# Performance work log

Hardware: AMD Instinct MI355X
Metric: run time of the kernel (lower is better)

## Reference

```python
import jax, jax.numpy as jnp
import numpy as np

D_MODEL = 1024
NUM_HEADS = 16
HEAD_DIM = D_MODEL // NUM_HEADS
B, S = 2, 2048


def setup_inputs() -> dict:
    key = jax.random.key(0)
    ks = jax.random.split(key, 10)
    sc = 1.0 / np.sqrt(D_MODEL)
    return {
        "x": jax.random.normal(ks[0], (B, S, D_MODEL), jnp.float32),
        "y": jax.random.normal(ks[1], (B, S, D_MODEL), jnp.float32),
        "Wkv": jax.random.normal(ks[2], (D_MODEL, 2 * D_MODEL), jnp.float32) * sc,
        "bkv": jax.random.normal(ks[3], (2 * D_MODEL,), jnp.float32) * 0.01,
        "Wq": jax.random.normal(ks[4], (D_MODEL, D_MODEL), jnp.float32) * sc,
        "bq": jax.random.normal(ks[5], (D_MODEL,), jnp.float32) * 0.01,
        "Wo": jax.random.normal(ks[6], (D_MODEL, D_MODEL), jnp.float32) * sc,
        "bo": jax.random.normal(ks[7], (D_MODEL,), jnp.float32) * 0.01,
    }


def reference(x, y, Wkv, bkv, Wq, bq, Wo, bo):
    b, s, d = x.shape
    # projections: kv from x (keys/values come from encoder side), q from y
    kv = x @ Wkv + bkv                      # [B, S, 2*d_model]
    q = y @ Wq + bq                         # [B, S, d_model]
    kv = kv.reshape(b, s, NUM_HEADS, 2 * HEAD_DIM).transpose(0, 2, 1, 3)  # [B,H,S,2*hd]
    q = q.reshape(b, s, NUM_HEADS, HEAD_DIM).transpose(0, 2, 1, 3)        # [B,H,S,hd]
    k, v = jnp.split(kv, 2, axis=-1)        # each [B,H,S,hd]
    scaled = jnp.einsum("bhqd,bhkd->bhqk", q, k) / np.sqrt(HEAD_DIM)      # [B,H,S,S]
    attention = jax.nn.softmax(scaled, axis=-1)
    values = jnp.einsum("bhqk,bhkd->bhqd", attention, v)                  # [B,H,S,hd]
    values = values.transpose(0, 2, 1, 3).reshape(b, s, d)                # [B,S,d_model]
    return values @ Wo + bo
```

## Files before the change

### kernel.cpp

```cpp
#include <hip/hip_runtime.h>
#include <hip/hip_bf16.h>

typedef __attribute__((ext_vector_type(8))) short short8;
typedef __attribute__((ext_vector_type(4))) short short4v;
typedef __attribute__((ext_vector_type(4))) float f32x4;
typedef __attribute__((ext_vector_type(16))) float f32x16;

#define B_  2
#define S_  2048
#define H_  16
#define HD_ 64
#define D_  1024
#define QSCALE 0.18033688f

__device__ __forceinline__ short f2bs(float f) {
  union { float f; unsigned u; } c; c.f = f;
  unsigned u = c.u;
  u += 0x7fffu + ((u >> 16) & 1u);
  return (short)(u >> 16);
}

__device__ __forceinline__ unsigned pack_bf16(float a, float b) {
  __hip_bfloat162 h = __float22bfloat162_rn(float2{a, b});
  return *reinterpret_cast<unsigned*>(&h);
}

__device__ __forceinline__ float fexp2(float x) {
#if __has_builtin(__builtin_amdgcn_exp2f)
  return __builtin_amdgcn_exp2f(x);
#else
  return exp2f(x);
#endif
}

__device__ __forceinline__ float frcp(float x) {
#if __has_builtin(__builtin_amdgcn_rcpf)
  return __builtin_amdgcn_rcpf(x);
#else
  return 1.0f / x;
#endif
}

#define GL2LDS(gp, lp) __builtin_amdgcn_global_load_lds( \
    (const __attribute__((address_space(1))) unsigned int*)(gp), \
    (__attribute__((address_space(3))) unsigned int*)(lp), 16, 0, 0)

__global__ __launch_bounds__(256)
void prep_kernel(const float* __restrict__ x, const float* __restrict__ y,
                 short* __restrict__ xb, short* __restrict__ yb,
                 const float* __restrict__ Wkv, short* __restrict__ Wkvt,
                 const float* __restrict__ Wq, short* __restrict__ Wqt,
                 const float* __restrict__ Wo, short* __restrict__ Wot) {
  __shared__ float tile[64][65];
  int bx = blockIdx.x;
  if (bx < 8192) {
    int i = bx * 256 + threadIdx.x;
    const float4* src; short4v* dst; int j;
    if (i < (1 << 20)) { src = (const float4*)x; dst = (short4v*)xb; j = i; }
    else               { src = (const float4*)y; dst = (short4v*)yb; j = i - (1 << 20); }
    float4 f = src[j];
    short4v o;
    o.x = f2bs(f.x); o.y = f2bs(f.y); o.z = f2bs(f.z); o.w = f2bs(f.w);
    dst[j] = o;
    return;
  }
  bx -= 8192;
  const float* in; short* out; int C, c0, r0;
  if (bx < 512)      { in = Wkv; out = Wkvt; C = 2048; c0 = (bx & 31) * 64; r0 = (bx >> 5) * 64; }
  else if (bx < 768) { bx -= 512; in = Wq; out = Wqt; C = 1024; c0 = (bx & 15) * 64; r0 = (bx >> 4) * 64; }
  else               { bx -= 768; in = Wo; out = Wot; C = 1024; c0 = (bx & 15) * 64; r0 = (bx >> 4) * 64; }
  const int tx = threadIdx.x & 63, ty = threadIdx.x >> 6;
#pragma unroll
  for (int i = 0; i < 16; ++i) {
    int r = ty + i * 4;
    tile[r][tx] = in[(size_t)(r0 + r) * C + c0 + tx];
  }
  __syncthreads();
#pragma unroll
  for (int i = 0; i < 16; ++i) {
    int r = ty + i * 4;
    out[(size_t)(c0 + r) * 1024 + r0 + tx] = f2bs(tile[tx][r]);
  }
}

template <int MODE>
__device__ __forceinline__ void gemm_body(const short* __restrict__ A, const short* __restrict__ Bt,
                                          const float* __restrict__ bias,
                                          void* __restrict__ out0, void* __restrict__ out1,
                                          int m0, int n0, int K, short* smem) {
  short* As_ = smem;
  short* Bs_ = smem + 8192;
  const int tid = threadIdx.x;
  const int w = tid >> 6, lane = tid & 63;
  const int q15 = lane & 15, quad = lane >> 4;
  const int wm = (w >> 1) * 64, wn = (w & 1) * 64;

  f32x4 acc[4][4];
#pragma unroll
  for (int i = 0; i < 4; ++i)
#pragma unroll
    for (int j = 0; j < 4; ++j) acc[i][j] = f32x4{0.f, 0.f, 0.f, 0.f};

  const int srow = w * 16 + (lane >> 2);
  const int gch  = (lane & 3) ^ ((lane >> 3) & 3);
  const short* Ag = A + (size_t)(m0 + srow) * K + gch * 8;
  const short* Bg = Bt + (size_t)(n0 + srow) * K + gch * 8;
  const int lof = srow * 32 + (lane & 3) * 8;

  GL2LDS(Ag,                  As_ + lof);
  GL2LDS(Ag + (size_t)64 * K, As_ + lof + 2048);
  GL2LDS(Bg,                  Bs_ + lof);
  GL2LDS(Bg + (size_t)64 * K, Bs_ + lof + 2048);

  const int NT = K >> 5;
  for (int kt = 0; kt < NT; ++kt) {
    __syncthreads();
    const short* Ac = As_ + (kt & 1) * 4096;
    const short* Bc = Bs_ + (kt & 1) * 4096;
    if (kt + 1 < NT) {
      const short* a2 = Ag + (size_t)(kt + 1) * 32;
      const short* b2 = Bg + (size_t)(kt + 1) * 32;
      short* ad = As_ + ((kt & 1) ^ 1) * 4096 + lof;
      short* bd = Bs_ + ((kt & 1) ^ 1) * 4096 + lof;
      GL2LDS(a2,                  ad);
      GL2LDS(a2 + (size_t)64 * K, ad + 2048);
      GL2LDS(b2,                  bd);
      GL2LDS(b2 + (size_t)64 * K, bd + 2048);
    }
    short8 af[4], bf[4];
#pragma unroll
    for (int mi = 0; mi < 4; ++mi) {
      int rr = wm + mi * 16 + q15;
      af[mi] = *(const short8*)(Ac + rr * 32 + ((quad ^ ((rr >> 1) & 3)) * 8));
    }
#pragma unroll
    for (int ni = 0; ni < 4; ++ni) {
      int rr = wn + ni * 16 + q15;
      bf[ni] = *(const short8*)(Bc + rr * 32 + ((quad ^ ((rr >> 1) & 3)) * 8));
    }
#pragma unroll
    for (int mi = 0; mi < 4; ++mi)
#pragma unroll
      for (int ni = 0; ni < 4; ++ni)
        acc[mi][ni] = __builtin_amdgcn_mfma_f32_16x16x32_bf16(af[mi], bf[ni], acc[mi][ni], 0, 0, 0);
  }
  __syncthreads();

  if constexpr (MODE == 0) {
#pragma unroll
    for (int mi = 0; mi < 4; ++mi)
#pragma unroll
      for (int ni = 0; ni < 4; ++ni) {
        const int n = n0 + wn + ni * 16 + q15;
        const float bn = bias[n];
#pragma unroll
        for (int r = 0; r < 4; ++r) {
          const int m = m0 + wm + mi * 16 + quad * 4 + r;
          int b = m >> 11, s = m & 2047, hh = n >> 6, d = n & 63;
          ((short*)out0)[((size_t)((b * H_ + hh) * S_ + s) << 6) + d] = f2bs((acc[mi][ni][r] + bn) * QSCALE);
        }
      }
  } else {
    const int hh = n0 >> 7;
    const int bb = m0 >> 11;
    const size_t bh = (size_t)(bb * H_ + hh);
    const int s0 = m0 & 2047;
    if ((w & 1) == 0) {
#pragma unroll
      for (int mi = 0; mi < 4; ++mi)
#pragma unroll
        for (int ni = 0; ni < 4; ++ni) {
          const float bn = bias[n0 + ni * 16 + q15];
#pragma unroll
          for (int r = 0; r < 4; ++r) {
            const int s = s0 + wm + mi * 16 + quad * 4 + r;
            ((short*)out0)[((bh * S_ + s) << 6) + ni * 16 + q15] = f2bs(acc[mi][ni][r] + bn);
          }
        }
    } else {
      short* VT = smem;
#pragma unroll
      for (int mi = 0; mi < 4; ++mi)
#pragma unroll
        for (int ni = 0; ni < 4; ++ni) {
          const int d = ni * 16 + q15;
          const float bn = bias[n0 + 64 + ni * 16 + q15];
#pragma unroll
          for (int t = 0; t < 2; ++t) {
            const int chunk = (wm >> 1) + mi * 8 + quad * 2 + t;
            unsigned pk = pack_bf16(acc[mi][ni][2 * t] + bn, acc[mi][ni][2 * t + 1] + bn);
            *reinterpret_cast<unsigned*>(VT + d * 128 + ((chunk ^ (d & 15)) * 2)) = pk;
          }
        }
    }
    __syncthreads();
    {
      short* VT = smem;
      const int d = tid >> 2, t4 = tid & 3;
      unsigned vals[16];
#pragma unroll
      for (int c = 0; c < 16; ++c) {
        int chunk = t4 * 16 + c;
        vals[c] = *reinterpret_cast<unsigned*>(VT + d * 128 + ((chunk ^ (d & 15)) * 2));
      }
      uint4* dst = (uint4*)((short*)out1 + ((bh * HD_ + d) << 11) + s0 + t4 * 32);
      dst[0] = uint4{vals[0], vals[1], vals[4],  vals[5]};
      dst[1] = uint4{vals[2], vals[3], vals[6],  vals[7]};
      dst[2] = uint4{vals[8], vals[9], vals[12], vals[13]};
      dst[3] = uint4{vals[10], vals[11], vals[14], vals[15]};
    }
  }
}

__global__ __launch_bounds__(256)
void proj_kernel(const short* __restrict__ xb, const short* __restrict__ Wkvt,
                 const float* __restrict__ bkv, short* __restrict__ Kb, short* __restrict__ Vtb,
                 const short* __restrict__ yb, const short* __restrict__ Wqt,
                 const float* __restrict__ bq, short* __restrict__ Qb) {
  __shared__ __align__(16) short smem[16384];
  int bx = blockIdx.x;
  bx = (bx & 7) * 96 + (bx >> 3);
  if (bx < 512)
    gemm_body<1>(xb, Wkvt, bkv, Kb, Vtb, (bx >> 4) * 128, (bx & 15) * 128, 1024, smem);
  else {
    bx -= 512;
    gemm_body<0>(yb, Wqt, bq, Qb, nullptr, (bx >> 3) * 128, (bx & 7) * 128, 1024, smem);
  }
}

__global__ __launch_bounds__(256)
void gemm_o_kernel(const short* __restrict__ A, const short* __restrict__ Bt,
                   const float* __restrict__ bias, float* __restrict__ out) {
  __shared__ __align__(16) short lds[16384];
  const int tid = threadIdx.x;
  const int w = tid >> 6, lane = tid & 63;
  const int q15 = lane & 15, quad = lane >> 4;
  const int m0 = blockIdx.y * 64, n0 = blockIdx.x * 64;
  const int wm = (w >> 1) * 32, wn = (w & 1) * 32;
  const int xw = q15 & 7;

  f32x4 acc[2][2];
#pragma unroll
  for (int i = 0; i < 2; ++i)
#pragma unroll
    for (int j = 0; j < 2; ++j) acc[i][j] = f32x4{0.f, 0.f, 0.f, 0.f};

  const int srow = w * 8 + (lane >> 3);
  const int gch  = (lane & 7) ^ (srow & 7);
  const int loff = w * 512 + lane * 8;
  const short* Ag = A + (size_t)(m0 + srow) * 1024 + gch * 8;
  const short* Bg = Bt + (size_t)(n0 + srow) * 1024 + gch * 8;

  GL2LDS(Ag,             lds + loff);
  GL2LDS(Ag + 32 * 1024, lds + loff + 2048);
  GL2LDS(Bg,             lds + 8192 + loff);
  GL2LDS(Bg + 32 * 1024, lds + 8192 + loff + 2048);

  for (int kt = 0; kt < 16; ++kt) {
    __syncthreads();
    const short* Ac = lds + ((kt & 1) ? 4096 : 0);
    const short* Bc = lds + 8192 + ((kt & 1) ? 4096 : 0);
    if (kt < 15) {
      const short* a2 = Ag + (kt + 1) * 64;
      const short* b2 = Bg + (kt + 1) * 64;
      short* ad = lds + ((kt & 1) ? 0 : 4096) + loff;
      short* bd = lds + 8192 + ((kt & 1) ? 0 : 4096) + loff;
      GL2LDS(a2,             ad);
      GL2LDS(a2 + 32 * 1024, ad + 2048);
      GL2LDS(b2,             bd);
      GL2LDS(b2 + 32 * 1024, bd + 2048);
    }
    short8 af[2][2], bf[2][2];
#pragma unroll
    for (int mi = 0; mi < 2; ++mi)
#pragma unroll
      for (int kk = 0; kk < 2; ++kk)
        af[mi][kk] = *(const short8*)(Ac + (wm + mi * 16 + q15) * 64 + (((kk * 4 + quad) ^ xw) * 8));
#pragma unroll
    for (int ni = 0; ni < 2; ++ni)
#pragma unroll
      for (int kk = 0; kk < 2; ++kk)
        bf[ni][kk] = *(const short8*)(Bc + (wn + ni * 16 + q15) * 64 + (((kk * 4 + quad) ^ xw) * 8));
#pragma unroll
    for (int mi = 0; mi < 2; ++mi)
#pragma unroll
      for (int ni = 0; ni < 2; ++ni)
#pragma unroll
        for (int kk = 0; kk < 2; ++kk)
          acc[mi][ni] = __builtin_amdgcn_mfma_f32_16x16x32_bf16(af[mi][kk], bf[ni][kk], acc[mi][ni], 0, 0, 0);
  }

#pragma unroll
  for (int mi = 0; mi < 2; ++mi)
#pragma unroll
    for (int ni = 0; ni < 2; ++ni) {
      const int n = n0 + wn + ni * 16 + q15;
      const float bn = bias[n];
#pragma unroll
      for (int r = 0; r < 4; ++r) {
        const int m = m0 + wm + mi * 16 + quad * 4 + r;
        out[(size_t)m * 1024 + n] = acc[mi][ni][r] + bn;
      }
    }
}

__global__ __launch_bounds__(256, 3)
void attn_kernel(const short* __restrict__ Q, const short* __restrict__ K,
                 const short* __restrict__ Vt, short* __restrict__ Out) {
  __shared__ __align__(16) short lds[24576];
  short* QP = lds + 16384;
  const int tid = threadIdx.x;
  const int w = tid >> 6, lane = tid & 63;
  const int l31 = lane & 31, h5 = lane >> 5;
  const int rsw = l31 & 7;
  const int bx = blockIdx.x;
  const int xcd = bx & 7, slot = bx >> 3;
  const int pp = xcd * 4 + (slot >> 4);
  const int qt = slot & 15;
  const int h = pp & 15, b = pp >> 4;
  const size_t bh = (size_t)(b * H_ + h);
  const short* Qg = Q + bh * (S_ * HD_) + qt * (128 * HD_);
  const short* Kg = K + bh * (S_ * HD_);
  const short* Vg = Vt + bh * (HD_ * S_);

  const int srow = tid >> 3;
  const int gch  = (tid & 7) ^ (srow & 7);
  const int loff = tid * 8;

  {
    const short* qg = Qg + srow * 64 + gch * 8;
#pragma unroll
    for (int t = 0; t < 4; ++t) GL2LDS(qg + t * 2048, QP + loff + t * 2048);
  }
  const short* kg = Kg + srow * 64 + gch * 8;
  const short* vg = Vg + (size_t)srow * S_ + gch * 8;
  GL2LDS(kg,                   lds + loff);
  GL2LDS(kg + 2048,            lds + loff + 2048);
  GL2LDS(vg,                   lds + 8192 + loff);
  GL2LDS(vg + (size_t)32 * S_, lds + 8192 + loff + 2048);
  __syncthreads();

  short8 aq[4];
#pragma unroll
  for (int kk = 0; kk < 4; ++kk)
    aq[kk] = *(const short8*)(QP + (w * 32 + l31) * 64 + (((kk * 2 + h5) ^ rsw) * 8));

  f32x16 oacc[2];
#pragma unroll
  for (int i = 0; i < 16; ++i) { oacc[0][i] = 0.f; oacc[1][i] = 0.f; }
  float lsum = 0.f;
  f32x16 z16;
#pragma unroll
  for (int i = 0; i < 16; ++i) z16[i] = 0.f;

  for (int kt = 0; kt < 32; ++kt) {
    __syncthreads();
    const short* Kc = lds + ((kt & 1) ? 4096 : 0);
    const short* Vc = lds + 8192 + ((kt & 1) ? 4096 : 0);
    if (kt < 31) {
      const short* k2 = kg + (kt + 1) * 4096;
      const short* v2 = vg + (kt + 1) * 64;
      short* kd = lds + ((kt & 1) ? 0 : 4096) + loff;
      short* vd = lds + 8192 + ((kt & 1) ? 0 : 4096) + loff;
      GL2LDS(k2,                   kd);
      GL2LDS(k2 + 2048,            kd + 2048);
      GL2LDS(v2,                   vd);
      GL2LDS(v2 + (size_t)32 * S_, vd + 2048);
    }

    f32x16 sacc[2];
    __builtin_amdgcn_s_setprio(1);
#pragma unroll
    for (int sb = 0; sb < 2; ++sb) {
      const short* kr = Kc + (sb * 32 + l31) * 64;
      short8 k0 = *(const short8*)(kr + (((0 + h5) ^ rsw) * 8));
      short8 k1 = *(const short8*)(kr + (((2 + h5) ^ rsw) * 8));
      short8 k2 = *(const short8*)(kr + (((4 + h5) ^ rsw) * 8));
      short8 k3 = *(const short8*)(kr + (((6 + h5) ^ rsw) * 8));
      f32x16 s = __builtin_amdgcn_mfma_f32_32x32x16_bf16(k0, aq[0], z16, 0, 0, 0);
      s = __builtin_amdgcn_mfma_f32_32x32x16_bf16(k1, aq[1], s, 0, 0, 0);
      s = __builtin_amdgcn_mfma_f32_32x32x16_bf16(k2, aq[2], s, 0, 0, 0);
      s = __builtin_amdgcn_mfma_f32_32x32x16_bf16(k3, aq[3], s, 0, 0, 0);
      sacc[sb] = s;
    }
    __builtin_amdgcn_s_setprio(0);

    short8 ap[4];
#pragma unroll
    for (int sb = 0; sb < 2; ++sb) {
      float e[16];
#pragma unroll
      for (int i = 0; i < 16; ++i) e[i] = fexp2(sacc[sb][i]);
      lsum += (((e[0] + e[1]) + (e[2] + e[3])) + ((e[4] + e[5]) + (e[6] + e[7])))
            + (((e[8] + e[9]) + (e[10] + e[11])) + ((e[12] + e[13]) + (e[14] + e[15])));
      union { unsigned u[4]; short8 s8; } lo, hi;
      lo.u[0] = pack_bf16(e[0], e[1]);   lo.u[1] = pack_bf16(e[2], e[3]);
      lo.u[2] = pack_bf16(e[4], e[5]);   lo.u[3] = pack_bf16(e[6], e[7]);
      hi.u[0] = pack_bf16(e[8], e[9]);   hi.u[1] = pack_bf16(e[10], e[11]);
      hi.u[2] = pack_bf16(e[12], e[13]); hi.u[3] = pack_bf16(e[14], e[15]);
      ap[sb * 2 + 0] = lo.s8;
      ap[sb * 2 + 1] = hi.s8;
    }

    __builtin_amdgcn_s_setprio(1);
#pragma unroll
    for (int db = 0; db < 2; ++db) {
      const short* vr = Vc + (db * 32 + l31) * 64;
      short8 v0 = *(const short8*)(vr + (((0 + h5) ^ rsw) * 8));
      short8 v1 = *(const short8*)(vr + (((2 + h5) ^ rsw) * 8));
      short8 v2 = *(const short8*)(vr + (((4 + h5) ^ rsw) * 8));
      short8 v3 = *(const short8*)(vr + (((6 + h5) ^ rsw) * 8));
      f32x16 o = oacc[db];
      o = __builtin_amdgcn_mfma_f32_32x32x16_bf16(ap[0], v0, o, 0, 0, 0);
      o = __builtin_amdgcn_mfma_f32_32x32x16_bf16(ap[1], v1, o, 0, 0, 0);
      o = __builtin_amdgcn_mfma_f32_32x32x16_bf16(ap[2], v2, o, 0, 0, 0);
      o = __builtin_amdgcn_mfma_f32_32x32x16_bf16(ap[3], v3, o, 0, 0, 0);
      oacc[db] = o;
    }
    __builtin_amdgcn_s_setprio(0);
  }

  float lt = lsum + __shfl_xor(lsum, 32);
  float inv[16];
#pragma unroll
  for (int r = 0; r < 16; ++r)
    inv[r] = frcp(__shfl(lt, (r & 3) + 8 * (r >> 2) + 4 * h5, 64));
#pragma unroll
  for (int db = 0; db < 2; ++db) {
    const int col = h * HD_ + db * 32 + l31;
#pragma unroll
    for (int r = 0; r < 16; ++r) {
      const int m = b * S_ + qt * 128 + w * 32 + (r & 3) + 8 * (r >> 2) + 4 * h5;
      Out[(size_t)m * D_ + col] = f2bs(oacc[db][r] * inv[r]);
    }
  }
}

extern "C" void kernel_launch(void* const* d_in, const int* in_sizes, int n_in,
                              void* d_out, int out_size, void* d_ws, size_t ws_size,
                              hipStream_t stream) {
  const float* x   = (const float*)d_in[0];
  const float* y   = (const float*)d_in[1];
  const float* Wkv = (const float*)d_in[2];
  const float* bkv = (const float*)d_in[3];
  const float* Wq  = (const float*)d_in[4];
  const float* bq  = (const float*)d_in[5];
  const float* Wo  = (const float*)d_in[6];
  const float* bo  = (const float*)d_in[7];
  float* out = (float*)d_out;

  short* xb   = (short*)d_ws;
  short* yb   = xb + (4 << 20);
  short* Wkvt = yb + (4 << 20);
  short* Wqt  = Wkvt + (2 << 20);
  short* Wot  = Wqt + (1 << 20);
  short* Kb   = Wot + (1 << 20);
  short* Vtb  = Kb + (4 << 20);
  short* Qb   = Vtb + (4 << 20);
  short* AOb  = Qb + (4 << 20);

  prep_kernel<<<9216, 256, 0, stream>>>(x, y, xb, yb, Wkv, Wkvt, Wq, Wqt, Wo, Wot);
  proj_kernel<<<768, 256, 0, stream>>>(xb, Wkvt, bkv, Kb, Vtb, yb, Wqt, bq, Qb);
  attn_kernel<<<512, 256, 0, stream>>>(Qb, Kb, Vtb, AOb);
  gemm_o_kernel<<<dim3(16, 64), 256, 0, stream>>>(AOb, Wot, bo, out);
}
```

Baseline: 207.2 us.

## Triple-buffer LDS staging with explicit vmcnt waits in projection and attention

Both the projection GEMM and the attention kernel move from double to triple buffering of the async global-to-LDS loads. Tiles are prefetched two iterations ahead, and each step waits with a partial s_waitcnt vmcnt plus a pinned barrier instead of a full __syncthreads drain. This is meant to hide global-load latency behind MFMA work. In exchange, LDS use grows and the attention launch bound drops from 3 to 2 blocks per CU, so occupancy may be lower.

After: 192.8 us. 6.9% less time.

```diff
diff --git a/kernel.cpp b/kernel.cpp
--- a/kernel.cpp
+++ b/kernel.cpp
@@ -44,6 +44,11 @@
 #define GL2LDS(gp, lp) __builtin_amdgcn_global_load_lds( \
     (const __attribute__((address_space(1))) unsigned int*)(gp), \
     (__attribute__((address_space(3))) unsigned int*)(lp), 16, 0, 0)
+
+#define WAITCNT4  asm volatile("s_waitcnt vmcnt(4)" ::: "memory")
+#define WAITCNT8  asm volatile("s_waitcnt vmcnt(8)" ::: "memory")
+#define WAITCNT0  asm volatile("s_waitcnt vmcnt(0)" ::: "memory")
+#define BARRIER_PIN do { __builtin_amdgcn_s_barrier(); __builtin_amdgcn_sched_barrier(0); } while (0)
 
 __global__ __launch_bounds__(256)
 void prep_kernel(const float* __restrict__ x, const float* __restrict__ y,
@@ -89,7 +94,7 @@
                                           void* __restrict__ out0, void* __restrict__ out1,
                                           int m0, int n0, int K, short* smem) {
   short* As_ = smem;
-  short* Bs_ = smem + 8192;
+  short* Bs_ = smem + 12288;
   const int tid = threadIdx.x;
   const int w = tid >> 6, lane = tid & 63;
   const int q15 = lane & 15, quad = lane >> 4;
@@ -107,26 +112,27 @@
   const short* Bg = Bt + (size_t)(n0 + srow) * K + gch * 8;
   const int lof = srow * 32 + (lane & 3) * 8;
 
-  GL2LDS(Ag,                  As_ + lof);
-  GL2LDS(Ag + (size_t)64 * K, As_ + lof + 2048);
-  GL2LDS(Bg,                  Bs_ + lof);
-  GL2LDS(Bg + (size_t)64 * K, Bs_ + lof + 2048);
+#define STAGE_AB(t, buf) do { \
+    const short* a2 = Ag + (size_t)(t) * 32; \
+    const short* b2 = Bg + (size_t)(t) * 32; \
+    short* ad = As_ + (buf) * 4096 + lof; \
+    short* bd = Bs_ + (buf) * 4096 + lof; \
+    GL2LDS(a2,                  ad); \
+    GL2LDS(a2 + (size_t)64 * K, ad + 2048); \
+    GL2LDS(b2,                  bd); \
+    GL2LDS(b2 + (size_t)64 * K, bd + 2048); \
+  } while (0)
 
   const int NT = K >> 5;
+  STAGE_AB(0, 0);
+  STAGE_AB(1, 1);
+  int cb = 0, ib = 2;
   for (int kt = 0; kt < NT; ++kt) {
-    __syncthreads();
-    const short* Ac = As_ + (kt & 1) * 4096;
-    const short* Bc = Bs_ + (kt & 1) * 4096;
-    if (kt + 1 < NT) {
-      const short* a2 = Ag + (size_t)(kt + 1) * 32;
-      const short* b2 = Bg + (size_t)(kt + 1) * 32;
-      short* ad = As_ + ((kt & 1) ^ 1) * 4096 + lof;
-      short* bd = Bs_ + ((kt & 1) ^ 1) * 4096 + lof;
-      GL2LDS(a2,                  ad);
-      GL2LDS(a2 + (size_t)64 * K, ad + 2048);
-      GL2LDS(b2,                  bd);
-      GL2LDS(b2 + (size_t)64 * K, bd + 2048);
-    }
+    if (kt < NT - 1) WAITCNT4; else WAITCNT0;
+    BARRIER_PIN;
+    if (kt + 2 < NT) STAGE_AB(kt + 2, ib);
+    const short* Ac = As_ + cb * 4096;
+    const short* Bc = Bs_ + cb * 4096;
     short8 af[4], bf[4];
 #pragma unroll
     for (int mi = 0; mi < 4; ++mi) {
@@ -143,7 +149,10 @@
 #pragma unroll
       for (int ni = 0; ni < 4; ++ni)
         acc[mi][ni] = __builtin_amdgcn_mfma_f32_16x16x32_bf16(af[mi], bf[ni], acc[mi][ni], 0, 0, 0);
-  }
+    cb = (cb == 2) ? 0 : cb + 1;
+    ib = (ib == 2) ? 0 : ib + 1;
+  }
+#undef STAGE_AB
   __syncthreads();
 
   if constexpr (MODE == 0) {
@@ -217,7 +226,7 @@
                  const float* __restrict__ bkv, short* __restrict__ Kb, short* __restrict__ Vtb,
                  const short* __restrict__ yb, const short* __restrict__ Wqt,
                  const float* __restrict__ bq, short* __restrict__ Qb) {
-  __shared__ __align__(16) short smem[16384];
+  __shared__ __align__(16) short smem[24576];
   int bx = blockIdx.x;
   bx = (bx & 7) * 96 + (bx >> 3);
   if (bx < 512)
@@ -304,11 +313,11 @@
     }
 }
 
-__global__ __launch_bounds__(256, 3)
+__global__ __launch_bounds__(256, 2)
 void attn_kernel(const short* __restrict__ Q, const short* __restrict__ K,
                  const short* __restrict__ Vt, short* __restrict__ Out) {
-  __shared__ __align__(16) short lds[24576];
-  short* QP = lds + 16384;
+  __shared__ __align__(16) short lds[32768];
+  short* QP = lds + 24576;
   const int tid = threadIdx.x;
   const int w = tid >> 6, lane = tid & 63;
   const int l31 = lane & 31, h5 = lane >> 5;
@@ -327,18 +336,29 @@
   const int gch  = (tid & 7) ^ (srow & 7);
   const int loff = tid * 8;
 
+  const short* kg = Kg + srow * 64 + gch * 8;
+  const short* vg = Vg + (size_t)srow * S_ + gch * 8;
+
+#define STAGE_KV(t, buf) do { \
+    const short* k2 = kg + (size_t)(t) * 4096; \
+    const short* v2 = vg + (size_t)(t) * 64; \
+    short* kd = lds + (buf) * 4096 + loff; \
+    short* vd = lds + 12288 + (buf) * 4096 + loff; \
+    GL2LDS(k2,                   kd); \
+    GL2LDS(k2 + 2048,            kd + 2048); \
+    GL2LDS(v2,                   vd); \
+    GL2LDS(v2 + (size_t)32 * S_, vd + 2048); \
+  } while (0)
+
   {
     const short* qg = Qg + srow * 64 + gch * 8;
 #pragma unroll
     for (int t = 0; t < 4; ++t) GL2LDS(qg + t * 2048, QP + loff + t * 2048);
   }
-  const short* kg = Kg + srow * 64 + gch * 8;
-  const short* vg = Vg + (size_t)srow * S_ + gch * 8;
-  GL2LDS(kg,                   lds + loff);
-  GL2LDS(kg + 2048,            lds + loff + 2048);
-  GL2LDS(vg,                   lds + 8192 + loff);
-  GL2LDS(vg + (size_t)32 * S_, lds + 8192 + loff + 2048);
-  __syncthreads();
+  STAGE_KV(0, 0);
+  STAGE_KV(1, 1);
+  WAITCNT8;
+  BARRIER_PIN;
 
   short8 aq[4];
 #pragma unroll
@@ -353,20 +373,13 @@
 #pragma unroll
   for (int i = 0; i < 16; ++i) z16[i] = 0.f;
 
+  int cb = 0, ib = 2;
   for (int kt = 0; kt < 32; ++kt) {
-    __syncthreads();
-    const short* Kc = lds + ((kt & 1) ? 4096 : 0);
-    const short* Vc = lds + 8192 + ((kt & 1) ? 4096 : 0);
-    if (kt < 31) {
-      const short* k2 = kg + (kt + 1) * 4096;
-      const short* v2 = vg + (kt + 1) * 64;
-      short* kd = lds + ((kt & 1) ? 0 : 4096) + loff;
-      short* vd = lds + 8192 + ((kt & 1) ? 0 : 4096) + loff;
-      GL2LDS(k2,                   kd);
-      GL2LDS(k2 + 2048,            kd + 2048);
-      GL2LDS(v2,                   vd);
-      GL2LDS(v2 + (size_t)32 * S_, vd + 2048);
-    }
+    if (kt < 31) WAITCNT4; else WAITCNT0;
+    BARRIER_PIN;
+    if (kt + 2 < 32) STAGE_KV(kt + 2, ib);
+    const short* Kc = lds + cb * 4096;
+    const short* Vc = lds + 12288 + cb * 4096;
 
     f32x16 sacc[2];
     __builtin_amdgcn_s_setprio(1);
@@ -418,7 +431,10 @@
       oacc[db] = o;
     }
     __builtin_amdgcn_s_setprio(0);
-  }
+    cb = (cb == 2) ? 0 : cb + 1;
+    ib = (ib == 2) ? 0 : ib + 1;
+  }
+#undef STAGE_KV
 
   float lt = lsum + __shfl_xor(lsum, 32);
   float inv[16];
```
